# Kernel optimization log

Measured on AMD Instinct MI355X. Metric: run time of the kernel, lower is better.

Reference implementation:

```python
import jax, jax.numpy as jnp
import numpy as np

B, S, D, H = 8, 4096, 512, 8
DK = D // H
DFF = 2 * D
KS = 3          # depthwise conv kernel size
EPS = 1e-6      # linear attention eps
LN_EPS = 1e-5


def setup_inputs() -> dict:
    key = jax.random.key(0)
    ks = jax.random.split(key, 24)
    w = lambda k, shape, s=0.02: (jax.random.normal(k, shape) * s).astype(jnp.float32)
    return {
        "x": jax.random.normal(ks[0], (B, S, D), dtype=jnp.float32),
        # q/k/v/o projections (torch Linear: y = x @ W.T + b, W is [out, in])
        "wq": w(ks[1], (D, D)), "bq": w(ks[2], (D,)),
        "wk": w(ks[3], (D, D)), "bk": w(ks[4], (D,)),
        "wv": w(ks[5], (D, D)), "bv": w(ks[6], (D,)),
        "wo": w(ks[7], (D, D)), "bo": w(ks[8], (D,)),
        # depthwise spatial convs on head_dim channels, weight [DK, KS], bias [DK]
        "qcw": w(ks[9], (DK, KS)), "qcb": w(ks[10], (DK,)),
        "kcw": w(ks[11], (DK, KS)), "kcb": w(ks[12], (DK,)),
        "vcw": w(ks[13], (DK, KS)), "vcb": w(ks[14], (DK,)),
        # conv-FFN 1x1 convs == linears, W1 [DFF, D], W2 [D, DFF]
        "w1": w(ks[15], (DFF, D)), "b1": w(ks[16], (DFF,)),
        "w2": w(ks[17], (D, DFF)), "b2": w(ks[18], (D,)),
        # layer norms
        "ln1_g": jnp.ones((D,), jnp.float32), "ln1_b": jnp.zeros((D,), jnp.float32),
        "ln2_g": jnp.ones((D,), jnp.float32), "ln2_b": jnp.zeros((D,), jnp.float32),
    }


def _sdwc(x, w, b):
    # x: [B, S, H, DK]; causal depthwise conv over seq per channel
    # (torch pads both sides by KS-1 then trims the last KS-1 => left pad only)
    s = x.shape[1]
    xp = jnp.pad(x, ((0, 0), (KS - 1, 0), (0, 0), (0, 0)))
    y = sum(xp[:, j:j + s] * w[:, j] for j in range(KS))
    return y + b


def _ln(x, g, b):
    m = jnp.mean(x, axis=-1, keepdims=True)
    v = jnp.mean((x - m) ** 2, axis=-1, keepdims=True)
    return (x - m) * jax.lax.rsqrt(v + LN_EPS) * g + b


def reference(x, wq, bq, wk, bk, wv, bv, qcw, qcb, kcw, kcb, vcw, vcb,
              wo, bo, w1, b1, w2, b2, ln1_g, ln1_b, ln2_g, ln2_b):
    b_, s_, _ = x.shape
    q = (jnp.einsum('bsd,od->bso', x, wq) + bq).reshape(b_, s_, H, DK)
    k = (jnp.einsum('bsd,od->bso', x, wk) + bk).reshape(b_, s_, H, DK)
    v = (jnp.einsum('bsd,od->bso', x, wv) + bv).reshape(b_, s_, H, DK)
    # depthwise spatial conv + elu(x)+1 feature map on q, k
    q = jax.nn.elu(_sdwc(q, qcw, qcb)) + 1.0
    k = jax.nn.elu(_sdwc(k, kcw, kcb)) + 1.0
    v = _sdwc(v, vcw, vcb)
    # linear attention in [B, H, S, DK]
    Q = q.transpose(0, 2, 1, 3)
    K = k.transpose(0, 2, 1, 3)
    V = v.transpose(0, 2, 1, 3)
    KV = jnp.einsum('bhsd,bhse->bhde', K, V)                       # [B,H,DK,DK]
    Z = 1.0 / jnp.einsum('bhsd,bhd->bhs', Q, K.sum(axis=2) + EPS)  # [B,H,S]
    Vn = jnp.einsum('bhde,bhsd,bhs->bhse', KV, Q, Z)               # [B,H,S,DK]
    attn = Vn.transpose(0, 2, 1, 3).reshape(b_, s_, D)
    attn = jnp.einsum('bsd,od->bso', attn, wo) + bo
    x = _ln(x + attn, ln1_g, ln1_b)
    # conv-FFN with squared (exact) GELU; dropout is identity at eval
    h = jnp.einsum('bsd,cd->bsc', x, w1) + b1
    g = jax.nn.gelu(h, approximate=False)
    h = g * g
    h = jnp.einsum('bsc,dc->bsd', h, w2) + b2
    return _ln(x + h, ln2_g, ln2_b)
```

## Files before the change

kernel.cpp:

```cpp
#include <hip/hip_runtime.h>
#include <hip/hip_bf16.h>
#include <math.h>

#define B_ 8
#define S_ 4096
#define D_ 512
#define H_ 8
#define DK_ 64
#define DFF_ 1024
#define SPLIT_ 16
#define KVSZ_ 4160
#define EPS_ 1e-6f
#define LN_EPS_ 1e-5f

typedef __attribute__((ext_vector_type(8))) short bf16x8;
typedef __attribute__((ext_vector_type(4))) float f32x4;

static __device__ __forceinline__ float b2f(unsigned short u) {
  unsigned int x = ((unsigned int)u) << 16;
  return __builtin_bit_cast(float, x);
}
static __device__ __forceinline__ unsigned short f2b(float f) {
  unsigned int u = __builtin_bit_cast(unsigned int, f);
  u += 0x7FFFu + ((u >> 16) & 1u);
  return (unsigned short)(u >> 16);
}

__global__ __launch_bounds__(256) void cvt_f32_bf16(
    const float* __restrict__ in, unsigned short* __restrict__ out, int n8)
{
  const int i = blockIdx.x * 256 + threadIdx.x;
  if (i >= n8) return;
  f32x4 a = ((const f32x4*)in)[i * 2];
  f32x4 b = ((const f32x4*)in)[i * 2 + 1];
  bf16x8 o;
  #pragma unroll
  for (int e = 0; e < 4; ++e) { o[e] = (short)f2b(a[e]); o[e + 4] = (short)f2b(b[e]); }
  ((bf16x8*)out)[i] = o;
}

__global__ __launch_bounds__(256) void cvt_weights(
    const float* __restrict__ wq, const float* __restrict__ wk,
    const float* __restrict__ wv, const float* __restrict__ wo,
    const float* __restrict__ w1, const float* __restrict__ w2,
    const float* __restrict__ bq, const float* __restrict__ bk,
    const float* __restrict__ bv,
    unsigned short* __restrict__ wb, float* __restrict__ bqkv)
{
  const int i = blockIdx.x * 256 + threadIdx.x;
  const float* src; int rel;
  if (i < 65536)       { src = (i < 32768)  ? wq : wk; rel = i & 32767; }
  else if (i < 131072) { src = (i < 98304)  ? wv : wo; rel = (i - 65536) & 32767; }
  else                 { src = (i < 196608) ? w1 : w2; rel = (i - 131072) & 65535; }
  f32x4 a = ((const f32x4*)src)[rel * 2];
  f32x4 b = ((const f32x4*)src)[rel * 2 + 1];
  bf16x8 o;
  #pragma unroll
  for (int e = 0; e < 4; ++e) { o[e] = (short)f2b(a[e]); o[e + 4] = (short)f2b(b[e]); }
  ((bf16x8*)wb)[i] = o;
  if (i < 1536) bqkv[i] = (i < 512) ? bq[i] : (i < 1024 ? bk[i - 512] : bv[i - 1024]);
}

template<int EPI>
__global__ __launch_bounds__(256) void gemm_bt(
    const unsigned short* __restrict__ A,
    const unsigned short* __restrict__ W,
    const float* __restrict__ bias,
    unsigned short* __restrict__ C,
    int M, int N, int K, int ntx)
{
  __shared__ unsigned short sA[128 * 32];
  __shared__ unsigned short sB[128 * 32];
  const int t = threadIdx.x;
  const int wave = t >> 6;
  const int lane = t & 63;
  const int bid = blockIdx.x;
  const int logical = (bid & 7) * ((int)gridDim.x >> 3) + (bid >> 3);
  const int row0 = (logical / ntx) << 7;
  const int col0 = (logical % ntx) << 7;

  f32x4 acc[4][4] = {};

  const int srow = t >> 2;
  const int scol = (t & 3) << 3;
  const unsigned short* ga = A + (size_t)(row0 + srow) * K + scol;
  const unsigned short* gb = W + (size_t)(col0 + srow) * K + scol;

  const int wm = (wave >> 1) << 6;
  const int wn = (wave & 1) << 6;
  const int fr = lane & 15;
  const int fk = (lane >> 4) << 3;

  for (int kt = 0; kt < K; kt += 32) {
    __builtin_amdgcn_global_load_lds(
        (const __attribute__((address_space(1))) void*)(ga + kt),
        (__attribute__((address_space(3))) void*)(sA + wave * 512), 16, 0, 0);
    __builtin_amdgcn_global_load_lds(
        (const __attribute__((address_space(1))) void*)(ga + (size_t)64 * K + kt),
        (__attribute__((address_space(3))) void*)(sA + 2048 + wave * 512), 16, 0, 0);
    __builtin_amdgcn_global_load_lds(
        (const __attribute__((address_space(1))) void*)(gb + kt),
        (__attribute__((address_space(3))) void*)(sB + wave * 512), 16, 0, 0);
    __builtin_amdgcn_global_load_lds(
        (const __attribute__((address_space(1))) void*)(gb + (size_t)64 * K + kt),
        (__attribute__((address_space(3))) void*)(sB + 2048 + wave * 512), 16, 0, 0);
    __syncthreads();

    bf16x8 af[4], bfr[4];
    #pragma unroll
    for (int i = 0; i < 4; ++i) {
      af[i]  = *(const bf16x8*)(sA + (wm + i * 16 + fr) * 32 + fk);
      bfr[i] = *(const bf16x8*)(sB + (wn + i * 16 + fr) * 32 + fk);
    }
    #pragma unroll
    for (int i = 0; i < 4; ++i)
      #pragma unroll
      for (int j = 0; j < 4; ++j)
        acc[i][j] = __builtin_amdgcn_mfma_f32_16x16x32_bf16(af[i], bfr[j], acc[i][j], 0, 0, 0);
    __syncthreads();
  }

  const int crow0 = row0 + wm + ((lane >> 4) << 2);
  const int ccol0 = col0 + wn + fr;
  unsigned short* Cb = C;
  if (EPI == 2) Cb = C + (size_t)(col0 >> 9) * M * 512;
  const int cstride = (EPI == 2) ? 512 : N;
  #pragma unroll
  for (int j = 0; j < 4; ++j) {
    const int col = ccol0 + j * 16;
    const float bv = bias[col];
    const int lcol = (EPI == 2) ? (col & 511) : col;
    #pragma unroll
    for (int i = 0; i < 4; ++i) {
      #pragma unroll
      for (int r = 0; r < 4; ++r) {
        float v = acc[i][j][r] + bv;
        if (EPI == 1) {
          float g = 0.5f * v * (1.0f + erff(v * 0.70710678118654752f));
          v = g * g;
        }
        Cb[(size_t)(crow0 + i * 16 + r) * cstride + lcol] = f2b(v);
      }
    }
  }
}

template<bool ELUP1>
__global__ __launch_bounds__(256) void dwconv(
    const unsigned short* __restrict__ in,
    const float* __restrict__ cw,
    const float* __restrict__ cb,
    unsigned short* __restrict__ out)
{
  const int vid = blockIdx.x * 256 + threadIdx.x;
  const int d8 = vid & 63;
  const int bs = vid >> 6;
  const int s  = bs & (S_ - 1);
  const int d0 = d8 << 3;
  const int dk0 = d0 & 63;

  float acc[8], wf[3][8];
  #pragma unroll
  for (int i = 0; i < 8; ++i) acc[i] = cb[dk0 + i];
  #pragma unroll
  for (int j = 0; j < 3; ++j)
    #pragma unroll
    for (int i = 0; i < 8; ++i) wf[j][i] = cw[(dk0 + i) * 3 + j];

  const size_t base = (size_t)bs * D_ + d0;
  #pragma unroll
  for (int j = 0; j < 3; ++j) {
    const int sr = s - 2 + j;
    if (sr >= 0) {
      bf16x8 xv = *(const bf16x8*)(in + base - (size_t)(2 - j) * D_);
      #pragma unroll
      for (int i = 0; i < 8; ++i) acc[i] += wf[j][i] * b2f((unsigned short)xv[i]);
    }
  }
  bf16x8 ov;
  #pragma unroll
  for (int i = 0; i < 8; ++i) {
    float v = acc[i];
    if (ELUP1) v = (v > 0.0f) ? (v + 1.0f) : expf(v);
    ov[i] = (short)f2b(v);
  }
  *(bf16x8*)(out + base) = ov;
}

__global__ __launch_bounds__(256) void kv_partial(
    const unsigned short* __restrict__ kf,
    const unsigned short* __restrict__ vf,
    float* __restrict__ part)
{
  __shared__ unsigned short kc[16 * 64];
  __shared__ float vc[16 * 64];
  const int t = threadIdx.x;
  const int bh = blockIdx.x;
  const int b = bh >> 3, h = bh & 7;
  const int s0 = blockIdx.y * (S_ / SPLIT_);
  const int d = t >> 2;
  const int e0 = (t & 3) << 4;
  const int lr = (t & 127) >> 3;
  const int lc = (t & 7) << 3;

  float acc[16] = {};
  float ksum = 0.0f;

  for (int chunk = 0; chunk < S_ / SPLIT_; chunk += 16) {
    const size_t g = ((size_t)(b * S_ + s0 + chunk + lr)) * D_ + h * 64 + lc;
    if (t < 128) {
      *(bf16x8*)(kc + lr * 64 + lc) = *(const bf16x8*)(kf + g);
    } else {
      bf16x8 vv = *(const bf16x8*)(vf + g);
      #pragma unroll
      for (int i = 0; i < 8; ++i) vc[lr * 64 + lc + i] = b2f((unsigned short)vv[i]);
    }
    __syncthreads();
    #pragma unroll 4
    for (int ss = 0; ss < 16; ++ss) {
      const float kd = b2f(kc[ss * 64 + d]);
      ksum += kd;
      #pragma unroll
      for (int j = 0; j < 16; ++j) acc[j] += kd * vc[ss * 64 + e0 + j];
    }
    __syncthreads();
  }
  float* dst = part + ((size_t)bh * SPLIT_ + blockIdx.y) * KVSZ_;
  #pragma unroll
  for (int j = 0; j < 16; ++j) dst[d * 64 + e0 + j] = acc[j];
  if ((t & 3) == 0) dst[4096 + d] = ksum;
}

__global__ __launch_bounds__(256) void kv_finalize(
    const float* __restrict__ part, float* __restrict__ fin)
{
  const int bh = blockIdx.x;
  for (int idx = threadIdx.x; idx < KVSZ_; idx += 256) {
    float s = 0.0f;
    for (int p = 0; p < SPLIT_; ++p) s += part[((size_t)bh * SPLIT_ + p) * KVSZ_ + idx];
    if (idx >= 4096) s += EPS_;
    fin[(size_t)bh * KVSZ_ + idx] = s;
  }
}

__global__ __launch_bounds__(256) void attn_out(
    const unsigned short* __restrict__ qf,
    const float* __restrict__ fin,
    unsigned short* __restrict__ attn)
{
  __shared__ float kv[64 * 64];
  __shared__ float ks[64];
  const int t = threadIdx.x;
  const int bh = blockIdx.x, b = bh >> 3, h = bh & 7;
  const int s = blockIdx.y * 64 + (t >> 2);
  const int e0 = (t & 3) << 4;

  const float* src = fin + (size_t)bh * KVSZ_;
  for (int i = t; i < 4096; i += 256) kv[i] = src[i];
  if (t < 64) ks[t] = src[4096 + t];
  __syncthreads();

  const unsigned short* qrow = qf + ((size_t)(b * S_ + s)) * D_ + h * 64;
  float q[64];
  #pragma unroll
  for (int i = 0; i < 8; ++i) {
    bf16x8 qv = *(const bf16x8*)(qrow + i * 8);
    #pragma unroll
    for (int k = 0; k < 8; ++k) q[i * 8 + k] = b2f((unsigned short)qv[k]);
  }
  float zden = 0.0f;
  #pragma unroll
  for (int dd = 0; dd < 64; ++dd) zden += q[dd] * ks[dd];
  const float z = 1.0f / zden;

  float acc[16] = {};
  for (int dd = 0; dd < 64; ++dd) {
    const float qd = q[dd];
    #pragma unroll
    for (int j = 0; j < 16; ++j) acc[j] += qd * kv[dd * 64 + e0 + j];
  }
  unsigned short* orow = attn + ((size_t)(b * S_ + s)) * D_ + h * 64 + e0;
  bf16x8 o0, o1;
  #pragma unroll
  for (int j = 0; j < 8; ++j) { o0[j] = (short)f2b(acc[j] * z); o1[j] = (short)f2b(acc[8 + j] * z); }
  *(bf16x8*)(orow) = o0;
  *(bf16x8*)(orow + 8) = o1;
}

template<bool AF32, bool OF32>
__global__ __launch_bounds__(256) void ln_add(
    const void* __restrict__ xa_,
    const unsigned short* __restrict__ xb,
    const float* __restrict__ gg,
    const float* __restrict__ bb,
    void* __restrict__ out_)
{
  const int t = threadIdx.x, lane = t & 63, w = t >> 6;
  const size_t row = (size_t)blockIdx.x * 4 + w;
  const size_t base = row * D_ + lane * 8;

  float v[8];
  if (AF32) {
    const float* xa = (const float*)xa_;
    f32x4 a0 = *(const f32x4*)(xa + base);
    f32x4 a1 = *(const f32x4*)(xa + base + 4);
    #pragma unroll
    for (int i = 0; i < 4; ++i) { v[i] = a0[i]; v[i + 4] = a1[i]; }
  } else {
    bf16x8 a = *(const bf16x8*)((const unsigned short*)xa_ + base);
    #pragma unroll
    for (int i = 0; i < 8; ++i) v[i] = b2f((unsigned short)a[i]);
  }
  bf16x8 c = *(const bf16x8*)(xb + base);
  float sum = 0.0f;
  #pragma unroll
  for (int i = 0; i < 8; ++i) { v[i] += b2f((unsigned short)c[i]); sum += v[i]; }
  #pragma unroll
  for (int off = 1; off < 64; off <<= 1) sum += __shfl_xor(sum, off, 64);
  const float mean = sum * (1.0f / 512.0f);
  float sq = 0.0f;
  #pragma unroll
  for (int i = 0; i < 8; ++i) { const float dd = v[i] - mean; sq += dd * dd; }
  #pragma unroll
  for (int off = 1; off < 64; off <<= 1) sq += __shfl_xor(sq, off, 64);
  const float rstd = rsqrtf(sq * (1.0f / 512.0f) + LN_EPS_);

  if (OF32) {
    float* out = (float*)out_;
    f32x4 o0, o1;
    #pragma unroll
    for (int i = 0; i < 4; ++i) {
      o0[i] = (v[i] - mean) * rstd * gg[lane * 8 + i] + bb[lane * 8 + i];
      o1[i] = (v[i + 4] - mean) * rstd * gg[lane * 8 + i + 4] + bb[lane * 8 + i + 4];
    }
    *(f32x4*)(out + base) = o0;
    *(f32x4*)(out + base + 4) = o1;
  } else {
    unsigned short* out = (unsigned short*)out_;
    bf16x8 o;
    #pragma unroll
    for (int i = 0; i < 8; ++i)
      o[i] = (short)f2b((v[i] - mean) * rstd * gg[lane * 8 + i] + bb[lane * 8 + i]);
    *(bf16x8*)(out + base) = o;
  }
}

extern "C" void kernel_launch(void* const* d_in, const int* in_sizes, int n_in,
                              void* d_out, int out_size, void* d_ws, size_t ws_size,
                              hipStream_t stream) {
  const float* x    = (const float*)d_in[0];
  const float* wq   = (const float*)d_in[1];
  const float* bq   = (const float*)d_in[2];
  const float* wk   = (const float*)d_in[3];
  const float* bk   = (const float*)d_in[4];
  const float* wv   = (const float*)d_in[5];
  const float* bv   = (const float*)d_in[6];
  const float* wo   = (const float*)d_in[7];
  const float* bo   = (const float*)d_in[8];
  const float* qcw  = (const float*)d_in[9];
  const float* qcb  = (const float*)d_in[10];
  const float* kcw  = (const float*)d_in[11];
  const float* kcb  = (const float*)d_in[12];
  const float* vcw  = (const float*)d_in[13];
  const float* vcb  = (const float*)d_in[14];
  const float* w1   = (const float*)d_in[15];
  const float* b1   = (const float*)d_in[16];
  const float* w2   = (const float*)d_in[17];
  const float* b2   = (const float*)d_in[18];
  const float* ln1g = (const float*)d_in[19];
  const float* ln1b = (const float*)d_in[20];
  const float* ln2g = (const float*)d_in[21];
  const float* ln2b = (const float*)d_in[22];

  const size_t E = (size_t)B_ * S_ * D_;
  unsigned short* s0 = (unsigned short*)d_ws;
  unsigned short* s1 = s0 + E;
  unsigned short* s2 = s0 + 2 * E;
  unsigned short* s3 = s0 + 3 * E;
  float* part = (float*)s2;
  float* fin  = part + (size_t)64 * SPLIT_ * KVSZ_;

  unsigned short* wb = (unsigned short*)d_out;
  unsigned short* wqkv_b = wb;
  unsigned short* wo_b   = wb + 786432;
  unsigned short* w1_b   = wb + 1048576;
  unsigned short* w2_b   = wb + 1572864;
  float* bqkv = (float*)(wb + 2097152);

  const int M = B_ * S_;

  cvt_f32_bf16<<<(int)(E / 8 / 256), 256, 0, stream>>>(x, s3, (int)(E / 8));
  cvt_weights<<<1024, 256, 0, stream>>>(wq, wk, wv, wo, w1, w2, bq, bk, bv, wb, bqkv);

  gemm_bt<2><<<3072, 256, 0, stream>>>(s3, wqkv_b, bqkv, s0, M, 1536, D_, 12);
  dwconv<true ><<<M * 64 / 256, 256, 0, stream>>>(s0, qcw, qcb, s3);
  dwconv<true ><<<M * 64 / 256, 256, 0, stream>>>(s1, kcw, kcb, s0);
  dwconv<false><<<M * 64 / 256, 256, 0, stream>>>(s2, vcw, vcb, s1);
  kv_partial<<<dim3(B_ * H_, SPLIT_), 256, 0, stream>>>(s0, s1, part);
  kv_finalize<<<B_ * H_, 256, 0, stream>>>(part, fin);
  attn_out<<<dim3(B_ * H_, S_ / 64), 256, 0, stream>>>(s3, fin, s0);
  gemm_bt<0><<<1024, 256, 0, stream>>>(s0, wo_b, bo, s1, M, D_, D_, 4);
  ln_add<true, false><<<M / 4, 256, 0, stream>>>(x, s1, ln1g, ln1b, s3);
  gemm_bt<1><<<2048, 256, 0, stream>>>(s3, w1_b, b1, s0, M, DFF_, D_, 8);
  gemm_bt<0><<<1024, 256, 0, stream>>>(s0, w2_b, b2, s2, M, D_, DFF_, 4);
  ln_add<false, true><<<M / 4, 256, 0, stream>>>(s3, s2, ln2g, ln2b, d_out);
}
```

Before: 632.2 us.

## Double-buffer GEMM LDS stages and widen tiles to 128x256

The bf16 MFMA GEMM now prefetches the next K-slice into a second LDS buffer while computing the current one, which removes one barrier per iteration and overlaps global loads with MFMA. Each block now computes a 128x256 tile instead of 128x128, doubling register accumulators per wave (4x8 fragments) to improve A-tile reuse. Grids are halved to match. The change increases register and LDS pressure, which may lower occupancy, and halves the block count for the smaller GEMMs.

```diff
diff --git a/kernel.cpp b/kernel.cpp
--- a/kernel.cpp
+++ b/kernel.cpp
@@ -62,63 +62,78 @@
 }
 
 template<int EPI>
-__global__ __launch_bounds__(256) void gemm_bt(
+__global__ __launch_bounds__(256, 2) void gemm_bt(
     const unsigned short* __restrict__ A,
     const unsigned short* __restrict__ W,
     const float* __restrict__ bias,
     unsigned short* __restrict__ C,
     int M, int N, int K, int ntx)
 {
-  __shared__ unsigned short sA[128 * 32];
-  __shared__ unsigned short sB[128 * 32];
+  __shared__ unsigned short sA[2 * 128 * 32];
+  __shared__ unsigned short sB[2 * 256 * 32];
   const int t = threadIdx.x;
   const int wave = t >> 6;
   const int lane = t & 63;
   const int bid = blockIdx.x;
   const int logical = (bid & 7) * ((int)gridDim.x >> 3) + (bid >> 3);
   const int row0 = (logical / ntx) << 7;
-  const int col0 = (logical % ntx) << 7;
-
-  f32x4 acc[4][4] = {};
-
-  const int srow = t >> 2;
-  const int scol = (t & 3) << 3;
+  const int col0 = (logical % ntx) << 8;
+
+  f32x4 acc[4][8] = {};
+
+  const int srow = (wave << 4) + (lane >> 2);
+  const int scol = (lane & 3) << 3;
   const unsigned short* ga = A + (size_t)(row0 + srow) * K + scol;
   const unsigned short* gb = W + (size_t)(col0 + srow) * K + scol;
+  const int ldsoff = (wave << 9);
 
   const int wm = (wave >> 1) << 6;
-  const int wn = (wave & 1) << 6;
+  const int wn = (wave & 1) << 7;
   const int fr = lane & 15;
   const int fk = (lane >> 4) << 3;
 
+  #define STAGE(bufsel, kt)                                                     \
+    {                                                                           \
+      _Pragma("unroll")                                                         \
+      for (int i = 0; i < 2; ++i)                                               \
+        __builtin_amdgcn_global_load_lds(                                       \
+            (const __attribute__((address_space(1))) void*)(ga + (size_t)(i * 64) * K + (kt)), \
+            (__attribute__((address_space(3))) void*)(sA + (bufsel) * 4096 + i * 2048 + ldsoff), \
+            16, 0, 0);                                                          \
+      _Pragma("unroll")                                                         \
+      for (int i = 0; i < 4; ++i)                                               \
+        __builtin_amdgcn_global_load_lds(                                       \
+            (const __attribute__((address_space(1))) void*)(gb + (size_t)(i * 64) * K + (kt)), \
+            (__attribute__((address_space(3))) void*)(sB + (bufsel) * 8192 + i * 2048 + ldsoff), \
+            16, 0, 0);                                                          \
+    }
+
+  STAGE(0, 0);
+  __syncthreads();
+
+  int cur = 0;
   for (int kt = 0; kt < K; kt += 32) {
-    __builtin_amdgcn_global_load_lds(
-        (const __attribute__((address_space(1))) void*)(ga + kt),
-        (__attribute__((address_space(3))) void*)(sA + wave * 512), 16, 0, 0);
-    __builtin_amdgcn_global_load_lds(
-        (const __attribute__((address_space(1))) void*)(ga + (size_t)64 * K + kt),
-        (__attribute__((address_space(3))) void*)(sA + 2048 + wave * 512), 16, 0, 0);
-    __builtin_amdgcn_global_load_lds(
-        (const __attribute__((address_space(1))) void*)(gb + kt),
-        (__attribute__((address_space(3))) void*)(sB + wave * 512), 16, 0, 0);
-    __builtin_amdgcn_global_load_lds(
-        (const __attribute__((address_space(1))) void*)(gb + (size_t)64 * K + kt),
-        (__attribute__((address_space(3))) void*)(sB + 2048 + wave * 512), 16, 0, 0);
-    __syncthreads();
-
-    bf16x8 af[4], bfr[4];
-    #pragma unroll
-    for (int i = 0; i < 4; ++i) {
-      af[i]  = *(const bf16x8*)(sA + (wm + i * 16 + fr) * 32 + fk);
-      bfr[i] = *(const bf16x8*)(sB + (wn + i * 16 + fr) * 32 + fk);
-    }
+    if (kt + 32 < K) STAGE(cur ^ 1, kt + 32);
+
+    const unsigned short* pA = sA + cur * 4096;
+    const unsigned short* pB = sB + cur * 8192;
+    bf16x8 af[4], bfv[8];
+    #pragma unroll
+    for (int i = 0; i < 4; ++i)
+      af[i] = *(const bf16x8*)(pA + (wm + i * 16 + fr) * 32 + fk);
+    #pragma unroll
+    for (int j = 0; j < 8; ++j)
+      bfv[j] = *(const bf16x8*)(pB + (wn + j * 16 + fr) * 32 + fk);
     #pragma unroll
     for (int i = 0; i < 4; ++i)
       #pragma unroll
-      for (int j = 0; j < 4; ++j)
-        acc[i][j] = __builtin_amdgcn_mfma_f32_16x16x32_bf16(af[i], bfr[j], acc[i][j], 0, 0, 0);
+      for (int j = 0; j < 8; ++j)
+        acc[i][j] = __builtin_amdgcn_mfma_f32_16x16x32_bf16(af[i], bfv[j], acc[i][j], 0, 0, 0);
+
     __syncthreads();
-  }
+    cur ^= 1;
+  }
+  #undef STAGE
 
   const int crow0 = row0 + wm + ((lane >> 4) << 2);
   const int ccol0 = col0 + wn + fr;
@@ -126,7 +141,7 @@
   if (EPI == 2) Cb = C + (size_t)(col0 >> 9) * M * 512;
   const int cstride = (EPI == 2) ? 512 : N;
   #pragma unroll
-  for (int j = 0; j < 4; ++j) {
+  for (int j = 0; j < 8; ++j) {
     const int col = ccol0 + j * 16;
     const float bv = bias[col];
     const int lcol = (EPI == 2) ? (col & 511) : col;
@@ -392,16 +407,16 @@
   cvt_f32_bf16<<<(int)(E / 8 / 256), 256, 0, stream>>>(x, s3, (int)(E / 8));
   cvt_weights<<<1024, 256, 0, stream>>>(wq, wk, wv, wo, w1, w2, bq, bk, bv, wb, bqkv);
 
-  gemm_bt<2><<<3072, 256, 0, stream>>>(s3, wqkv_b, bqkv, s0, M, 1536, D_, 12);
+  gemm_bt<2><<<1536, 256, 0, stream>>>(s3, wqkv_b, bqkv, s0, M, 1536, D_, 6);
   dwconv<true ><<<M * 64 / 256, 256, 0, stream>>>(s0, qcw, qcb, s3);
   dwconv<true ><<<M * 64 / 256, 256, 0, stream>>>(s1, kcw, kcb, s0);
   dwconv<false><<<M * 64 / 256, 256, 0, stream>>>(s2, vcw, vcb, s1);
   kv_partial<<<dim3(B_ * H_, SPLIT_), 256, 0, stream>>>(s0, s1, part);
   kv_finalize<<<B_ * H_, 256, 0, stream>>>(part, fin);
   attn_out<<<dim3(B_ * H_, S_ / 64), 256, 0, stream>>>(s3, fin, s0);
-  gemm_bt<0><<<1024, 256, 0, stream>>>(s0, wo_b, bo, s1, M, D_, D_, 4);
+  gemm_bt<0><<<512, 256, 0, stream>>>(s0, wo_b, bo, s1, M, D_, D_, 2);
   ln_add<true, false><<<M / 4, 256, 0, stream>>>(x, s1, ln1g, ln1b, s3);
-  gemm_bt<1><<<2048, 256, 0, stream>>>(s3, w1_b, b1, s0, M, DFF_, D_, 8);
-  gemm_bt<0><<<1024, 256, 0, stream>>>(s0, w2_b, b2, s2, M, D_, DFF_, 4);
+  gemm_bt<1><<<1024, 256, 0, stream>>>(s3, w1_b, b1, s0, M, DFF_, D_, 4);
+  gemm_bt<0><<<512, 256, 0, stream>>>(s0, w2_b, b2, s2, M, D_, DFF_, 2);
   ln_add<false, true><<<M / 4, 256, 0, stream>>>(s3, s2, ln2g, ln2b, d_out);
 }
```

After: 601.9 us. -4.8%, faster.

## Replace 128x128 GEMM with 256x256 double-buffered 8-wave pipelined kernel

Applied to the files above, without the earlier changes.

Replaces the simple 128x128 tile, single-buffered bf16 GEMM with a 256x256 tile, 512-thread kernel that uses K-tiles of 64 and double-buffers LDS. Global-to-LDS loads are issued asynchronously and interleaved with the MFMA quadrants. LDS rows use an XOR swizzle to avoid bank conflicts, and setprio raises MFMA priority. The aim is to raise operand reuse and overlap memory with compute. In exchange it uses 128KB of LDS per block, needs large register tiles, and launches fewer blocks (256 for the D=512 outputs, which is about one wave over the CUs).

```diff
diff --git a/kernel.cpp b/kernel.cpp
--- a/kernel.cpp
+++ b/kernel.cpp
@@ -62,84 +62,138 @@
 }
 
 template<int EPI>
-__global__ __launch_bounds__(256) void gemm_bt(
+__global__ __launch_bounds__(512, 2) void gemm8p(
     const unsigned short* __restrict__ A,
-    const unsigned short* __restrict__ W,
+    const unsigned short* __restrict__ Wm,
     const float* __restrict__ bias,
     unsigned short* __restrict__ C,
     int M, int N, int K, int ntx)
 {
-  __shared__ unsigned short sA[128 * 32];
-  __shared__ unsigned short sB[128 * 32];
+  __shared__ unsigned short sA[2][16384];
+  __shared__ unsigned short sB[2][16384];
   const int t = threadIdx.x;
-  const int wave = t >> 6;
-  const int lane = t & 63;
-  const int bid = blockIdx.x;
-  const int logical = (bid & 7) * ((int)gridDim.x >> 3) + (bid >> 3);
-  const int row0 = (logical / ntx) << 7;
-  const int col0 = (logical % ntx) << 7;
-
-  f32x4 acc[4][4] = {};
-
-  const int srow = t >> 2;
-  const int scol = (t & 3) << 3;
-  const unsigned short* ga = A + (size_t)(row0 + srow) * K + scol;
-  const unsigned short* gb = W + (size_t)(col0 + srow) * K + scol;
-
-  const int wm = (wave >> 1) << 6;
-  const int wn = (wave & 1) << 6;
+  const int wave = t >> 6, lane = t & 63;
+  const int logical = ((int)blockIdx.x & 7) * ((int)gridDim.x >> 3) + ((int)blockIdx.x >> 3);
+  const int row0 = (logical / ntx) << 8;
+  const int col0 = (logical % ntx) << 8;
+
+  const int mw = wave >> 2;
+  const int nw = wave & 3;
   const int fr = lane & 15;
-  const int fk = (lane >> 4) << 3;
-
-  for (int kt = 0; kt < K; kt += 32) {
-    __builtin_amdgcn_global_load_lds(
-        (const __attribute__((address_space(1))) void*)(ga + kt),
-        (__attribute__((address_space(3))) void*)(sA + wave * 512), 16, 0, 0);
-    __builtin_amdgcn_global_load_lds(
-        (const __attribute__((address_space(1))) void*)(ga + (size_t)64 * K + kt),
-        (__attribute__((address_space(3))) void*)(sA + 2048 + wave * 512), 16, 0, 0);
-    __builtin_amdgcn_global_load_lds(
-        (const __attribute__((address_space(1))) void*)(gb + kt),
-        (__attribute__((address_space(3))) void*)(sB + wave * 512), 16, 0, 0);
-    __builtin_amdgcn_global_load_lds(
-        (const __attribute__((address_space(1))) void*)(gb + (size_t)64 * K + kt),
-        (__attribute__((address_space(3))) void*)(sB + 2048 + wave * 512), 16, 0, 0);
-    __syncthreads();
-
-    bf16x8 af[4], bfr[4];
-    #pragma unroll
-    for (int i = 0; i < 4; ++i) {
-      af[i]  = *(const bf16x8*)(sA + (wm + i * 16 + fr) * 32 + fk);
-      bfr[i] = *(const bf16x8*)(sB + (wn + i * 16 + fr) * 32 + fk);
-    }
-    #pragma unroll
-    for (int i = 0; i < 4; ++i)
-      #pragma unroll
-      for (int j = 0; j < 4; ++j)
-        acc[i][j] = __builtin_amdgcn_mfma_f32_16x16x32_bf16(af[i], bfr[j], acc[i][j], 0, 0, 0);
-    __syncthreads();
-  }
-
-  const int crow0 = row0 + wm + ((lane >> 4) << 2);
-  const int ccol0 = col0 + wn + fr;
+  const int g16 = (lane >> 4) << 4;
+
+  const unsigned short* gsrc[2][2][2];
+  #pragma unroll
+  for (int h = 0; h < 2; ++h)
+    #pragma unroll
+    for (int j = 0; j < 2; ++j) {
+      const int D    = h * 16384 + j * 8192 + t * 16;
+      const int prow = D >> 7;
+      const int cole = ((D & 127) ^ ((prow & 7) << 4)) >> 1;
+      const int ar = ((prow >> 6) & 1) * 128 + (prow >> 7) * 64 + (prow & 63);
+      const int br = ((prow & 127) >> 5) * 64 + (prow >> 7) * 32 + (prow & 31);
+      gsrc[0][h][j] = A  + (size_t)(row0 + ar) * K + cole;
+      gsrc[1][h][j] = Wm + (size_t)(col0 + br) * K + cole;
+    }
+
+#define STG(mat, slot, h, j, kt)                                               \
+  __builtin_amdgcn_global_load_lds(                                            \
+      (const __attribute__((address_space(1))) void*)(gsrc[mat][h][j] + (size_t)(kt) * 64), \
+      (__attribute__((address_space(3))) void*)(((mat) ? &sB[slot][0] : &sA[slot][0]) + (h) * 8192 + (j) * 4096 + wave * 512), \
+      16, 0, 0)
+
+  f32x4 acc[8][4] = {};
+  bf16x8 af[4][2], bf[2][2][2];
+
+#define RD_A(slot, mhalf)                                                      \
+  { _Pragma("unroll") for (int mfi = 0; mfi < 4; ++mfi)                        \
+      _Pragma("unroll") for (int ks = 0; ks < 2; ++ks) {                       \
+        const int lr = (mhalf) * 128 + mw * 64 + mfi * 16 + fr;                \
+        const int cb = (ks * 64 + g16) ^ ((lr & 7) << 4);                      \
+        af[mfi][ks] = *(const bf16x8*)((const char*)&sA[slot][0] + lr * 128 + cb); } }
+#define RD_B(slot, nhalf)                                                      \
+  { _Pragma("unroll") for (int nfi = 0; nfi < 2; ++nfi)                        \
+      _Pragma("unroll") for (int ks = 0; ks < 2; ++ks) {                       \
+        const int lr = (nhalf) * 128 + nw * 32 + nfi * 16 + fr;                \
+        const int cb = (ks * 64 + g16) ^ ((lr & 7) << 4);                      \
+        bf[nhalf][nfi][ks] = *(const bf16x8*)((const char*)&sB[slot][0] + lr * 128 + cb); } }
+#define MMQ(mhalf, nhalf)                                                      \
+  { __builtin_amdgcn_s_setprio(1);                                             \
+    _Pragma("unroll") for (int mfi = 0; mfi < 4; ++mfi)                        \
+      _Pragma("unroll") for (int nfi = 0; nfi < 2; ++nfi)                      \
+        _Pragma("unroll") for (int ks = 0; ks < 2; ++ks)                       \
+          acc[(mhalf)*4+mfi][(nhalf)*2+nfi] = __builtin_amdgcn_mfma_f32_16x16x32_bf16( \
+              af[mfi][ks], bf[nhalf][nfi][ks], acc[(mhalf)*4+mfi][(nhalf)*2+nfi], 0, 0, 0); \
+    __builtin_amdgcn_s_setprio(0); }
+#define BAR() __builtin_amdgcn_s_barrier()
+#define LGKM0() { asm volatile("s_waitcnt lgkmcnt(0)" ::: "memory"); __builtin_amdgcn_sched_barrier(0); }
+#define VMC(n)  asm volatile("s_waitcnt vmcnt(" #n ")" ::: "memory")
+
+  STG(0,0,0,0,0); STG(0,0,0,1,0); STG(0,0,1,0,0); STG(0,0,1,1,0);
+  STG(1,0,0,0,0); STG(1,0,0,1,0); STG(1,0,1,0,0); STG(1,0,1,1,0);
+  STG(0,1,0,0,1); STG(0,1,0,1,1); STG(0,1,1,0,1); STG(0,1,1,1,1);
+  STG(1,1,0,0,1); STG(1,1,0,1,1); STG(1,1,1,0,1); STG(1,1,1,1,1);
+  VMC(8);
+  BAR();
+
+  const int nt2 = K >> 7;
+  for (int i = 0; i < nt2; ++i) {
+    const bool st = (i + 1 < nt2);
+    const int k2 = 2 * i + 2, k3 = 2 * i + 3;
+    RD_A(0, 0); RD_B(0, 0);
+    BAR(); LGKM0(); MMQ(0, 0); BAR();
+    RD_B(0, 1);
+    if (st) { STG(0,0,0,0,k2); STG(0,0,0,1,k2); }
+    BAR(); LGKM0(); MMQ(0, 1); BAR();
+    RD_A(0, 1);
+    if (st) { STG(1,0,0,0,k2); STG(1,0,0,1,k2); }
+    BAR(); LGKM0(); MMQ(1, 0); BAR();
+    if (st) { STG(1,0,1,0,k2); STG(1,0,1,1,k2);
+              STG(0,0,1,0,k2); STG(0,0,1,1,k2);
+              VMC(8); }
+    else      VMC(0);
+    BAR(); MMQ(1, 1); BAR();
+    RD_A(1, 0); RD_B(1, 0);
+    BAR(); LGKM0(); MMQ(0, 0); BAR();
+    RD_B(1, 1);
+    if (st) { STG(0,1,0,0,k3); STG(0,1,0,1,k3); }
+    BAR(); LGKM0(); MMQ(0, 1); BAR();
+    RD_A(1, 1);
+    if (st) { STG(1,1,0,0,k3); STG(1,1,0,1,k3); }
+    BAR(); LGKM0(); MMQ(1, 0); BAR();
+    if (st) { STG(1,1,1,0,k3); STG(1,1,1,1,k3);
+              STG(0,1,1,0,k3); STG(0,1,1,1,k3);
+              VMC(8); }
+    BAR(); MMQ(1, 1); BAR();
+  }
+#undef STG
+#undef RD_A
+#undef RD_B
+#undef MMQ
+#undef BAR
+#undef LGKM0
+#undef VMC
+
+  const int crow0 = row0 + mw * 128 + ((lane >> 4) << 2);
+  const int ccol0 = col0 + nw * 64 + fr;
   unsigned short* Cb = C;
-  if (EPI == 2) Cb = C + (size_t)(col0 >> 9) * M * 512;
-  const int cstride = (EPI == 2) ? 512 : N;
-  #pragma unroll
-  for (int j = 0; j < 4; ++j) {
-    const int col = ccol0 + j * 16;
+  int cstr = N;
+  if (EPI == 2) { Cb = C + (size_t)(col0 >> 9) * M * 512; cstr = 512; }
+  #pragma unroll
+  for (int nf = 0; nf < 4; ++nf) {
+    const int col = ccol0 + nf * 16;
     const float bv = bias[col];
     const int lcol = (EPI == 2) ? (col & 511) : col;
     #pragma unroll
-    for (int i = 0; i < 4; ++i) {
+    for (int mf = 0; mf < 8; ++mf) {
       #pragma unroll
       for (int r = 0; r < 4; ++r) {
-        float v = acc[i][j][r] + bv;
+        float v = acc[mf][nf][r] + bv;
         if (EPI == 1) {
           float g = 0.5f * v * (1.0f + erff(v * 0.70710678118654752f));
           v = g * g;
         }
-        Cb[(size_t)(crow0 + i * 16 + r) * cstride + lcol] = f2b(v);
+        Cb[(size_t)(crow0 + mf * 16 + r) * cstr + lcol] = f2b(v);
       }
     }
   }
@@ -392,16 +446,16 @@
   cvt_f32_bf16<<<(int)(E / 8 / 256), 256, 0, stream>>>(x, s3, (int)(E / 8));
   cvt_weights<<<1024, 256, 0, stream>>>(wq, wk, wv, wo, w1, w2, bq, bk, bv, wb, bqkv);
 
-  gemm_bt<2><<<3072, 256, 0, stream>>>(s3, wqkv_b, bqkv, s0, M, 1536, D_, 12);
+  gemm8p<2><<<768, 512, 0, stream>>>(s3, wqkv_b, bqkv, s0, M, 1536, D_, 6);
   dwconv<true ><<<M * 64 / 256, 256, 0, stream>>>(s0, qcw, qcb, s3);
   dwconv<true ><<<M * 64 / 256, 256, 0, stream>>>(s1, kcw, kcb, s0);
   dwconv<false><<<M * 64 / 256, 256, 0, stream>>>(s2, vcw, vcb, s1);
   kv_partial<<<dim3(B_ * H_, SPLIT_), 256, 0, stream>>>(s0, s1, part);
   kv_finalize<<<B_ * H_, 256, 0, stream>>>(part, fin);
   attn_out<<<dim3(B_ * H_, S_ / 64), 256, 0, stream>>>(s3, fin, s0);
-  gemm_bt<0><<<1024, 256, 0, stream>>>(s0, wo_b, bo, s1, M, D_, D_, 4);
+  gemm8p<0><<<256, 512, 0, stream>>>(s0, wo_b, bo, s1, M, D_, D_, 2);
   ln_add<true, false><<<M / 4, 256, 0, stream>>>(x, s1, ln1g, ln1b, s3);
-  gemm_bt<1><<<2048, 256, 0, stream>>>(s3, w1_b, b1, s0, M, DFF_, D_, 8);
-  gemm_bt<0><<<1024, 256, 0, stream>>>(s0, w2_b, b2, s2, M, D_, DFF_, 4);
+  gemm8p<1><<<512, 512, 0, stream>>>(s3, w1_b, b1, s0, M, DFF_, D_, 4);
+  gemm8p<0><<<256, 512, 0, stream>>>(s0, w2_b, b2, s2, M, D_, DFF_, 2);
   ln_add<false, true><<<M / 4, 256, 0, stream>>>(s3, s2, ln2g, ln2b, d_out);
 }
```

After: 735.4 us. 1.16x slower.
